# Optimization experiments

Measured on AMD Instinct MI355X. Metric: run time of the kernel, lower is better.

The kernel has to match this reference:

```python
import jax, jax.numpy as jnp
import numpy as np

B, S, OUT = 128, 3000, 84
CODE_SEQ = 30
LAT = 1024
C, D = 128, 16
CB = C * D  # 2048
IN = CODE_SEQ * OUT  # 2520


def setup_inputs() -> dict:
    key = jax.random.key(0)
    ks = jax.random.split(key, 16)
    def w(k, shape):
        fan_in = shape[0]
        return (jax.random.normal(k, shape, dtype=jnp.float32) / np.sqrt(fan_in)).astype(jnp.float32)
    return {
        "y": jax.random.normal(ks[0], (B, S, OUT), dtype=jnp.float32),
        "emb": jax.random.uniform(ks[1], (C, D), minval=-1.0 / C, maxval=1.0 / C, dtype=jnp.float32),
        "eW1": w(ks[2], (IN, LAT)), "eb1": jnp.zeros((LAT,), jnp.float32),
        "eW2": w(ks[3], (LAT, LAT)), "eb2": jnp.zeros((LAT,), jnp.float32),
        "eW3": w(ks[4], (LAT, CB)), "eb3": jnp.zeros((CB,), jnp.float32),
        "dW1": w(ks[5], (CB, LAT)), "db1": jnp.zeros((LAT,), jnp.float32),
        "dW2": w(ks[6], (LAT, LAT)), "db2": jnp.zeros((LAT,), jnp.float32),
        "dW3": w(ks[7], (LAT, IN)), "db3": jnp.zeros((IN,), jnp.float32),
    }


def _mlp(z, W1, b1, W2, b2, W3, b3):
    # LinearEncoder in eval mode (dropout = identity): Linear->ELU->Linear->ELU->Linear
    z = jax.nn.elu(z @ W1 + b1)
    z = jax.nn.elu(z @ W2 + b2)
    return z @ W3 + b3


def reference(y, emb, eW1, eb1, eW2, eb2, eW3, eb3, dW1, db1, dW2, db2, dW3, db3):
    batch, seq_len = y.shape[0], y.shape[1]
    # seq_len % code_seq == 0 -> padding branch is a no-op
    y2 = y.reshape(batch, -1, IN)                 # (B, n_m, 2520)
    n_m = y2.shape[1]
    ze = _mlp(y2, eW1, eb1, eW2, eb2, eW3, eb3)   # (B, n_m, 2048)
    zef = ze.reshape(batch, n_m, -1, D)           # (B, n_m, G=128, 16)
    # squared L2 distance to each of C codes, without materializing (B,n_m,G,C,D)
    dist = (
        jnp.sum(zef ** 2, -1, keepdims=True)
        - 2.0 * jnp.einsum("bngd,cd->bngc", zef, emb)
        + jnp.sum(emb ** 2, -1)
    )                                             # (B, n_m, G, C)
    nn_idx = jnp.argmin(dist, -1)                 # (B, n_m, G)
    zq = emb[nn_idx].reshape(batch, n_m, -1)      # (B, n_m, 2048)
    dec_in = ze + jax.lax.stop_gradient(zq - ze)  # straight-through
    out = _mlp(dec_in, dW1, db1, dW2, db2, dW3, db3)
    out = out.reshape(batch, -1, OUT)[:, :seq_len, :]
    return (out, ze, zq)
```

## Files before the change

kernel.cpp:

```cpp
#include <hip/hip_runtime.h>
#include <hip/hip_bf16.h>
#include <cstdint>
#include <cstddef>

typedef __bf16 bf16_t;
typedef bf16_t bf16x8 __attribute__((ext_vector_type(8)));
typedef float  f32x4  __attribute__((ext_vector_type(4)));

__device__ __forceinline__ void gl_lds16(const void* g, void* l) {
  __builtin_amdgcn_global_load_lds(
      (const __attribute__((address_space(1))) void*)g,
      (__attribute__((address_space(3))) void*)l, 16, 0, 0);
}

#define BAR()  __builtin_amdgcn_s_barrier()
#define LGK0() asm volatile("s_waitcnt lgkmcnt(0)" ::: "memory")

__device__ __forceinline__ void transpose_tile(
    const float* __restrict__ W, bf16_t* __restrict__ Wt,
    int K, int N, int Kpad, int Npad, int bx, int by, int t)
{
  __shared__ float tile[32][33];
  const int tx = t & 31, ty = t >> 5;
  const int k0 = bx * 32, n0 = by * 32;
#pragma unroll
  for (int i = 0; i < 4; ++i) {
    int k = k0 + ty + i * 8, n = n0 + tx;
    tile[ty + i * 8][tx] = (k < K && n < N) ? W[(size_t)k * N + n] : 0.f;
  }
  __syncthreads();
#pragma unroll
  for (int i = 0; i < 4; ++i) {
    int n = n0 + ty + i * 8, k = k0 + tx;
    if (n < Npad && k < Kpad)
      Wt[(size_t)n * Kpad + k] = (bf16_t)tile[tx][ty + i * 8];
  }
}

__global__ __launch_bounds__(256) void prep_kernel(
    const float* __restrict__ y, bf16_t* __restrict__ X0,
    const float* __restrict__ eW1, bf16_t* __restrict__ W1t,
    const float* __restrict__ eW2, bf16_t* __restrict__ W2t,
    const float* __restrict__ eW3, bf16_t* __restrict__ W3t,
    const float* __restrict__ dW1, bf16_t* __restrict__ V1t,
    const float* __restrict__ dW2, bf16_t* __restrict__ V2t,
    const float* __restrict__ dW3, bf16_t* __restrict__ V3t)
{
  const int b = blockIdx.x;
  const int t = threadIdx.x;
  if (b < 16000) {
    const int idx = b * 256 + t;
    const int r = idx / 320, c = (idx % 320) * 8;
    bf16x8 v;
    if (c < 2520) {
      const float4 f0 = *(const float4*)(y + (size_t)r * 2520 + c);
      const float4 f1 = *(const float4*)(y + (size_t)r * 2520 + c + 4);
      v[0] = (bf16_t)f0.x; v[1] = (bf16_t)f0.y; v[2] = (bf16_t)f0.z; v[3] = (bf16_t)f0.w;
      v[4] = (bf16_t)f1.x; v[5] = (bf16_t)f1.y; v[6] = (bf16_t)f1.z; v[7] = (bf16_t)f1.w;
    } else {
#pragma unroll
      for (int j = 0; j < 8; ++j) v[j] = (bf16_t)0.f;
    }
    *(bf16x8*)(X0 + (size_t)r * 2560 + c) = v;
    return;
  }
  int lb = b - 16000;
  if (lb < 2560)      { transpose_tile(eW1, W1t, 2520, 1024, 2560, 1024, lb % 80, lb / 80, t); return; }
  lb -= 2560;
  if (lb < 1024)      { transpose_tile(eW2, W2t, 1024, 1024, 1024, 1024, lb % 32, lb / 32, t); return; }
  lb -= 1024;
  if (lb < 2048)      { transpose_tile(eW3, W3t, 1024, 2048, 1024, 2048, lb % 32, lb / 32, t); return; }
  lb -= 2048;
  if (lb < 2048)      { transpose_tile(dW1, V1t, 2048, 1024, 2048, 1024, lb % 64, lb / 64, t); return; }
  lb -= 2048;
  if (lb < 1024)      { transpose_tile(dW2, V2t, 1024, 1024, 1024, 1024, lb % 32, lb / 32, t); return; }
  lb -= 1024;
  transpose_tile(dW3, V3t, 1024, 2520, 1024, 2560, lb % 32, lb / 32, t);
}

template<int ELU>
__global__ __launch_bounds__(512, 4) void gemm128(
    const bf16_t* __restrict__ A, const bf16_t* __restrict__ Bt,
    const float* __restrict__ bias,
    bf16_t* __restrict__ Cb, float* __restrict__ Cf,
    int M, int N, int K, int Nlog)
{
  __shared__ __align__(16) bf16_t lds[36864];

  const int t  = threadIdx.x;
  const int w  = t >> 6, l = t & 63;
  const int fr = l & 15, kg = l >> 4;
  const int wm = (w >> 1) * 64, wn = (w & 1) * 64;

  const int gx = gridDim.x;
  const int nwg = gx * (int)gridDim.y;
  int lin = blockIdx.y * gx + blockIdx.x;
  int q8 = nwg >> 3, r8 = nwg & 7, xcd = lin & 7, idx = lin >> 3;
  int swz = (xcd < r8 ? xcd * (q8 + 1) : r8 * (q8 + 1) + (xcd - r8) * q8) + idx;
  const int tn = (swz % gx) * 128;
  const int tm = (swz / gx) * 256;

  const int srow = t >> 2;
  const int scol = (t & 3) * 8;
  const int sdst = t * 8;

  const int NT = K >> 5;

  f32x4 acc[4][4];
#pragma unroll
  for (int i = 0; i < 4; ++i)
#pragma unroll
    for (int j = 0; j < 4; ++j) acc[i][j] = (f32x4){0.f, 0.f, 0.f, 0.f};

  auto stage = [&](int slot, int kn) {
    bf16_t* d = lds + slot * 12288;
    gl_lds16(A  + (size_t)(tm + srow) * K + kn + scol,       d + sdst);
    gl_lds16(A  + (size_t)(tm + 128 + srow) * K + kn + scol, d + 4096 + sdst);
    gl_lds16(Bt + (size_t)(tn + srow) * K + kn + scol,       d + 8192 + sdst);
  };

  stage(0, 0);
  stage(1, 32);
  asm volatile("s_waitcnt vmcnt(3)" ::: "memory");
  BAR();

  for (int kt = 0; kt < NT; ++kt) {
    const int slot = kt % 3;
    const bf16_t* aH = lds + slot * 12288 + wm * 32;
    const bf16_t* bH = lds + slot * 12288 + 8192 + wn * 32;

    if (kt + 2 < NT) stage((kt + 2) % 3, (kt + 2) << 5);

    bf16x8 af[4], bf_[4];
#pragma unroll
    for (int mi = 0; mi < 4; ++mi)
      af[mi] = *(const bf16x8*)(aH + (mi * 16 + fr) * 32 + kg * 8);
#pragma unroll
    for (int nj = 0; nj < 4; ++nj)
      bf_[nj] = *(const bf16x8*)(bH + (nj * 16 + fr) * 32 + kg * 8);
    LGK0();
    __builtin_amdgcn_s_setprio(1);
#pragma unroll
    for (int mi = 0; mi < 4; ++mi)
#pragma unroll
      for (int nj = 0; nj < 4; ++nj)
        acc[mi][nj] = __builtin_amdgcn_mfma_f32_16x16x32_bf16(af[mi], bf_[nj], acc[mi][nj], 0, 0, 0);
    __builtin_amdgcn_s_setprio(0);
    asm volatile("s_waitcnt vmcnt(3)" ::: "memory");
    BAR();
  }

#pragma unroll
  for (int mi = 0; mi < 4; ++mi) {
    const int row0 = tm + wm + mi * 16 + kg * 4;
#pragma unroll
    for (int nj = 0; nj < 4; ++nj) {
      const int col = tn + wn + nj * 16 + fr;
      const float bv = (col < Nlog) ? bias[col] : 0.f;
#pragma unroll
      for (int r = 0; r < 4; ++r) {
        float v = acc[mi][nj][r] + bv;
        if (ELU) v = (v > 0.f) ? v : expm1f(v);
        const int row = row0 + r;
        if (Cb) Cb[(size_t)row * N + col] = (bf16_t)v;
        if (Cf && col < Nlog) Cf[(size_t)row * Nlog + col] = v;
      }
    }
  }
}

__global__ __launch_bounds__(256) void vq_mfma(
    const float* __restrict__ ze, const float* __restrict__ emb,
    float* __restrict__ zq, bf16_t* __restrict__ zqb)
{
  __shared__ float  se[2048];
  __shared__ bf16_t seb[2048];
  const int t = threadIdx.x;
  for (int i = t; i < 2048; i += 256) { float v = emb[i]; se[i] = v; seb[i] = (bf16_t)v; }
  __syncthreads();

  const int l = t & 63, w = t >> 6;
  const int col = l & 15;
  const int ks8 = (l >> 4) * 8;
  const bool kact = (ks8 < 16);

  bf16x8 bfrag[8];
  float  hv[8];
#pragma unroll
  for (int cb = 0; cb < 8; ++cb) {
    float s = 0.f;
    bf16x8 bf;
#pragma unroll
    for (int j = 0; j < 8; ++j) bf[j] = (bf16_t)0.f;
    if (kact) {
      const float* ep = se + (cb * 16 + col) * 16 + ks8;
      float4 e0 = *(const float4*)ep;
      float4 e1 = *(const float4*)(ep + 4);
      bf[0] = (bf16_t)e0.x; bf[1] = (bf16_t)e0.y; bf[2] = (bf16_t)e0.z; bf[3] = (bf16_t)e0.w;
      bf[4] = (bf16_t)e1.x; bf[5] = (bf16_t)e1.y; bf[6] = (bf16_t)e1.z; bf[7] = (bf16_t)e1.w;
      s = e0.x*e0.x + e0.y*e0.y + e0.z*e0.z + e0.w*e0.w
        + e1.x*e1.x + e1.y*e1.y + e1.z*e1.z + e1.w*e1.w;
    }
    s += __shfl_xor(s, 16);
    s += __shfl_xor(s, 32);
    bfrag[cb] = bf;
    hv[cb] = 0.5f * s;
  }

  const int base_tile = blockIdx.x * 64 + w * 16;
  for (int it = 0; it < 16; ++it) {
    const int tile = base_tile + it;
    const int row = tile >> 3, g0 = (tile & 7) * 16;

    bf16x8 afrag;
#pragma unroll
    for (int j = 0; j < 8; ++j) afrag[j] = (bf16_t)0.f;
    if (kact) {
      const float* ap = ze + (size_t)row * 2048 + (g0 + col) * 16 + ks8;
      float4 a0 = *(const float4*)ap;
      float4 a1 = *(const float4*)(ap + 4);
      afrag[0] = (bf16_t)(-a0.x); afrag[1] = (bf16_t)(-a0.y);
      afrag[2] = (bf16_t)(-a0.z); afrag[3] = (bf16_t)(-a0.w);
      afrag[4] = (bf16_t)(-a1.x); afrag[5] = (bf16_t)(-a1.y);
      afrag[6] = (bf16_t)(-a1.z); afrag[7] = (bf16_t)(-a1.w);
    }

    f32x4 dd[8];
#pragma unroll
    for (int cb = 0; cb < 8; ++cb) {
      f32x4 c = (f32x4){hv[cb], hv[cb], hv[cb], hv[cb]};
      dd[cb] = __builtin_amdgcn_mfma_f32_16x16x32_bf16(afrag, bfrag[cb], c, 0, 0, 0);
    }

#pragma unroll
    for (int r = 0; r < 4; ++r) {
      float bd = dd[0][r]; int bi = col;
#pragma unroll
      for (int cb = 1; cb < 8; ++cb) {
        float v = dd[cb][r];
        int   ci = cb * 16 + col;
        if (v < bd) { bd = v; bi = ci; }
      }
#pragma unroll
      for (int m = 1; m < 16; m <<= 1) {
        float od = __shfl_xor(bd, m);
        int   oi = __shfl_xor(bi, m);
        if (od < bd || (od == bd && oi < bi)) { bd = od; bi = oi; }
      }
      if (col == r) {
        const int tok = (l >> 4) * 4 + r;
        const size_t go = ((size_t)row * 128 + g0 + tok) * 16;
        const float*  e  = se  + bi * 16;
        const bf16_t* eb = seb + bi * 16;
#pragma unroll
        for (int v = 0; v < 4; ++v)
          *(float4*)(zq + go + v * 4) = ((const float4*)e)[v];
        *(bf16x8*)(zqb + go)     = ((const bf16x8*)eb)[0];
        *(bf16x8*)(zqb + go + 8) = ((const bf16x8*)eb)[1];
      }
    }
  }
}

extern "C" void kernel_launch(void* const* d_in, const int* in_sizes, int n_in,
                              void* d_out, int out_size, void* d_ws, size_t ws_size,
                              hipStream_t stream)
{
  const float* y   = (const float*)d_in[0];
  const float* emb = (const float*)d_in[1];
  const float* eW1 = (const float*)d_in[2];
  const float* eb1 = (const float*)d_in[3];
  const float* eW2 = (const float*)d_in[4];
  const float* eb2 = (const float*)d_in[5];
  const float* eW3 = (const float*)d_in[6];
  const float* eb3 = (const float*)d_in[7];
  const float* dW1 = (const float*)d_in[8];
  const float* db1 = (const float*)d_in[9];
  const float* dW2 = (const float*)d_in[10];
  const float* db2 = (const float*)d_in[11];
  const float* dW3 = (const float*)d_in[12];
  const float* db3 = (const float*)d_in[13];

  float* out = (float*)d_out;
  float* ze  = out + 32256000;
  float* zq  = ze + 26214400;

  uint8_t* ws = (uint8_t*)d_ws;
  size_t off = 0;
  auto alloc = [&](size_t bytes) -> void* {
    void* p = ws + off; off += (bytes + 255) & ~(size_t)255; return p;
  };
  bf16_t* X0  = (bf16_t*)alloc(12800ULL * 2560 * 2);
  bf16_t* W1t = (bf16_t*)alloc(1024ULL * 2560 * 2);
  bf16_t* W2t = (bf16_t*)alloc(1024ULL * 1024 * 2);
  bf16_t* W3t = (bf16_t*)alloc(2048ULL * 1024 * 2);
  bf16_t* V1t = (bf16_t*)alloc(1024ULL * 2048 * 2);
  bf16_t* V2t = (bf16_t*)alloc(1024ULL * 1024 * 2);
  bf16_t* V3t = (bf16_t*)alloc(2560ULL * 1024 * 2);
  bf16_t* H1  = (bf16_t*)alloc(12800ULL * 1024 * 2);
  bf16_t* H2  = (bf16_t*)alloc(12800ULL * 1024 * 2);
  bf16_t* ZQb = (bf16_t*)alloc(12800ULL * 2048 * 2);

  prep_kernel<<<27264, 256, 0, stream>>>(y, X0, eW1, W1t, eW2, W2t, eW3, W3t,
                                         dW1, V1t, dW2, V2t, dW3, V3t);

  gemm128<1><<<dim3(8, 50), 512, 0, stream>>>(X0, W1t, eb1, H1, nullptr, 12800, 1024, 2560, 1024);
  gemm128<1><<<dim3(8, 50), 512, 0, stream>>>(H1, W2t, eb2, H2, nullptr, 12800, 1024, 1024, 1024);
  gemm128<0><<<dim3(16, 50), 512, 0, stream>>>(H2, W3t, eb3, nullptr, ze, 12800, 2048, 1024, 2048);
  vq_mfma<<<1600, 256, 0, stream>>>(ze, emb, zq, ZQb);
  gemm128<1><<<dim3(8, 50), 512, 0, stream>>>(ZQb, V1t, db1, H1, nullptr, 12800, 1024, 2048, 1024);
  gemm128<1><<<dim3(8, 50), 512, 0, stream>>>(H1, V2t, db2, H2, nullptr, 12800, 1024, 1024, 1024);
  gemm128<0><<<dim3(20, 50), 512, 0, stream>>>(H2, V3t, db3, nullptr, out, 12800, 2560, 1024, 2520);
}
```

Measured before the change: 613.7 us.

## Load B fragments directly from global into registers, keep only A in LDS

The B (weight) tile is no longer staged through LDS. Each wave now loads its four B fragments straight from global memory into registers, one step ahead, interleaved between the MFMA groups, while A stays in a triple-buffered LDS ring. This cuts LDS footprint and LDS read traffic, which could raise occupancy. In exchange, global loads are uncoalesced (16-byte per-lane reads along K rows), and the vmcnt accounting mixes register loads with the LDS-direct loads. An early B load could stall the pipeline if its latency is not hidden.

```diff
diff --git a/kernel.cpp b/kernel.cpp
--- a/kernel.cpp
+++ b/kernel.cpp
@@ -14,7 +14,6 @@
 }
 
 #define BAR()  __builtin_amdgcn_s_barrier()
-#define LGK0() asm volatile("s_waitcnt lgkmcnt(0)" ::: "memory")
 
 __device__ __forceinline__ void transpose_tile(
     const float* __restrict__ W, bf16_t* __restrict__ Wt,
@@ -85,7 +84,7 @@
     bf16_t* __restrict__ Cb, float* __restrict__ Cf,
     int M, int N, int K, int Nlog)
 {
-  __shared__ __align__(16) bf16_t lds[36864];
+  __shared__ __align__(16) bf16_t lds[24576];
 
   const int t  = threadIdx.x;
   const int w  = t >> 6, l = t & 63;
@@ -112,41 +111,60 @@
 #pragma unroll
     for (int j = 0; j < 4; ++j) acc[i][j] = (f32x4){0.f, 0.f, 0.f, 0.f};
 
-  auto stage = [&](int slot, int kn) {
-    bf16_t* d = lds + slot * 12288;
-    gl_lds16(A  + (size_t)(tm + srow) * K + kn + scol,       d + sdst);
-    gl_lds16(A  + (size_t)(tm + 128 + srow) * K + kn + scol, d + 4096 + sdst);
-    gl_lds16(Bt + (size_t)(tn + srow) * K + kn + scol,       d + 8192 + sdst);
+  auto stageA = [&](int slot, int kn) {
+    bf16_t* d = lds + slot * 8192;
+    gl_lds16(A + (size_t)(tm + srow) * K + kn + scol,       d + sdst);
+    gl_lds16(A + (size_t)(tm + 128 + srow) * K + kn + scol, d + 4096 + sdst);
   };
 
-  stage(0, 0);
-  stage(1, 32);
-  asm volatile("s_waitcnt vmcnt(3)" ::: "memory");
+  const bf16_t* bp0 = Bt + (size_t)(tn + wn +  0 + fr) * K + kg * 8;
+  const bf16_t* bp1 = Bt + (size_t)(tn + wn + 16 + fr) * K + kg * 8;
+  const bf16_t* bp2 = Bt + (size_t)(tn + wn + 32 + fr) * K + kg * 8;
+  const bf16_t* bp3 = Bt + (size_t)(tn + wn + 48 + fr) * K + kg * 8;
+
+  bf16x8 bcur0, bcur1, bcur2, bcur3;
+
+  bcur0 = *(const bf16x8*)bp0; bp0 += 32;
+  bcur1 = *(const bf16x8*)bp1; bp1 += 32;
+  bcur2 = *(const bf16x8*)bp2; bp2 += 32;
+  bcur3 = *(const bf16x8*)bp3; bp3 += 32;
+  stageA(0, 0);
+  stageA(1, 32);
+  asm volatile("s_waitcnt vmcnt(0)" ::: "memory");
   BAR();
 
   for (int kt = 0; kt < NT; ++kt) {
     const int slot = kt % 3;
-    const bf16_t* aH = lds + slot * 12288 + wm * 32;
-    const bf16_t* bH = lds + slot * 12288 + 8192 + wn * 32;
-
-    if (kt + 2 < NT) stage((kt + 2) % 3, (kt + 2) << 5);
-
-    bf16x8 af[4], bf_[4];
+    const bf16_t* aH = lds + slot * 8192 + wm * 32;
+    const bool pfB = (kt + 1 < NT);
+
+    if (kt + 2 < NT) stageA((kt + 2) % 3, (kt + 2) << 5);
+
+    bf16x8 af[4];
+#pragma unroll
+    for (int q = 0; q < 4; ++q)
+      af[q] = *(const bf16x8*)(aH + (q * 16 + fr) * 32 + kg * 8);
+
+    __builtin_amdgcn_s_setprio(1);
 #pragma unroll
     for (int mi = 0; mi < 4; ++mi)
-      af[mi] = *(const bf16x8*)(aH + (mi * 16 + fr) * 32 + kg * 8);
-#pragma unroll
-    for (int nj = 0; nj < 4; ++nj)
-      bf_[nj] = *(const bf16x8*)(bH + (nj * 16 + fr) * 32 + kg * 8);
-    LGK0();
-    __builtin_amdgcn_s_setprio(1);
+      acc[mi][0] = __builtin_amdgcn_mfma_f32_16x16x32_bf16(af[mi], bcur0, acc[mi][0], 0, 0, 0);
+    if (pfB) { bcur0 = *(const bf16x8*)bp0; bp0 += 32; }
 #pragma unroll
     for (int mi = 0; mi < 4; ++mi)
-#pragma unroll
-      for (int nj = 0; nj < 4; ++nj)
-        acc[mi][nj] = __builtin_amdgcn_mfma_f32_16x16x32_bf16(af[mi], bf_[nj], acc[mi][nj], 0, 0, 0);
+      acc[mi][1] = __builtin_amdgcn_mfma_f32_16x16x32_bf16(af[mi], bcur1, acc[mi][1], 0, 0, 0);
+    if (pfB) { bcur1 = *(const bf16x8*)bp1; bp1 += 32; }
+#pragma unroll
+    for (int mi = 0; mi < 4; ++mi)
+      acc[mi][2] = __builtin_amdgcn_mfma_f32_16x16x32_bf16(af[mi], bcur2, acc[mi][2], 0, 0, 0);
+    if (pfB) { bcur2 = *(const bf16x8*)bp2; bp2 += 32; }
+#pragma unroll
+    for (int mi = 0; mi < 4; ++mi)
+      acc[mi][3] = __builtin_amdgcn_mfma_f32_16x16x32_bf16(af[mi], bcur3, acc[mi][3], 0, 0, 0);
+    if (pfB) { bcur3 = *(const bf16x8*)bp3; bp3 += 32; }
     __builtin_amdgcn_s_setprio(0);
-    asm volatile("s_waitcnt vmcnt(3)" ::: "memory");
+
+    asm volatile("s_waitcnt vmcnt(6)" ::: "memory");
     BAR();
   }
 
```

New measurement: 1.016 ms. 1.66x slower.
